# Kernel optimization log

Hardware: AMD Instinct MI355X
Metric: run time of the kernel (lower is better)

Reference implementation:

```python
import jax, jax.numpy as jnp
import numpy as np

B, T, D = 64, 512, 768
H = D // 2      # per-direction LSTM hidden
L = 33          # num_labels


def setup_inputs() -> dict:
    key = jax.random.key(0)
    ks = jax.random.split(key, 14)
    input_embed = jax.random.normal(ks[0], (B, T, D), dtype=jnp.float32)
    # pack_padded_sequence requires lengths sorted in decreasing order
    lengths = jnp.sort(jax.random.randint(ks[1], (B,), T // 2, T + 1))[::-1]
    lengths = lengths.at[0].set(T)
    mask = jnp.arange(T)[None, :] < lengths[:, None]          # [B,T] bool
    labels = jax.random.randint(ks[2], (B, T), 0, L, dtype=jnp.int32)
    index = jax.random.randint(ks[3], (B, 2), 0, T)
    s = 0.1
    w_ih_f = jax.random.normal(ks[4], (4 * H, D), jnp.float32) * s
    w_hh_f = jax.random.normal(ks[5], (4 * H, H), jnp.float32) * s
    b_f = jax.random.normal(ks[6], (4 * H,), jnp.float32) * s
    w_ih_b = jax.random.normal(ks[7], (4 * H, D), jnp.float32) * s
    w_hh_b = jax.random.normal(ks[8], (4 * H, H), jnp.float32) * s
    b_b = jax.random.normal(ks[9], (4 * H,), jnp.float32) * s
    lin_w = jax.random.normal(ks[10], (L, 2 * H), jnp.float32) * s
    lin_b = jnp.zeros((L,), jnp.float32)
    trans = jax.random.normal(ks[11], (L, L), jnp.float32) * s
    start_trans = jax.random.normal(ks[12], (L,), jnp.float32) * s
    end_trans = jax.random.normal(ks[13], (L,), jnp.float32) * s
    return dict(input_embed=input_embed, mask=mask, labels=labels, index=index,
                w_ih_f=w_ih_f, w_hh_f=w_hh_f, b_f=b_f,
                w_ih_b=w_ih_b, w_hh_b=w_hh_b, b_b=b_b,
                lin_w=lin_w, lin_b=lin_b,
                trans=trans, start_trans=start_trans, end_trans=end_trans)


def _run_lstm(x, mask_f, w_ih, w_hh, b):
    """Unidirectional LSTM over packed (length-masked) sequences.
    Output is zero at padded steps; state is frozen past each sequence length.
    x: [B,T,D] -> [B,T,H]. Torch gate order: i, f, g, o.
    """
    xp = jnp.einsum('btd,gd->btg', x, w_ih) + b          # [B,T,4H] precomputed
    xp_t = xp.transpose(1, 0, 2)                         # [T,B,4H]
    m_t = mask_f.T[:, :, None]                           # [T,B,1]
    nH = w_hh.shape[1]
    init = (jnp.zeros((x.shape[0], nH), x.dtype), jnp.zeros((x.shape[0], nH), x.dtype))

    def step(carry, inp):
        h, c = carry
        xg, m = inp
        g = xg + h @ w_hh.T
        i, f, gc, o = jnp.split(g, 4, axis=-1)
        c_new = jax.nn.sigmoid(f) * c + jax.nn.sigmoid(i) * jnp.tanh(gc)
        h_new = jax.nn.sigmoid(o) * jnp.tanh(c_new)
        carry = (jnp.where(m > 0, h_new, h), jnp.where(m > 0, c_new, c))
        return carry, h_new * m

    _, ys = jax.lax.scan(step, init, (xp_t, m_t))
    return ys.transpose(1, 0, 2)


def reference(input_embed, mask, labels, index,
              w_ih_f, w_hh_f, b_f, w_ih_b, w_hh_b, b_b,
              lin_w, lin_b, trans, start_trans, end_trans):
    mask_f = mask.astype(input_embed.dtype)              # [B,T]
    lengths = mask.sum(1).astype(jnp.int32)              # [B]

    # BiLSTM with pack_padded semantics (dropout in eval mode = identity)
    h_fwd = _run_lstm(input_embed, mask_f, w_ih_f, w_hh_f, b_f)
    # reverse within each sequence's valid region (involution on valid steps)
    rev_idx = jnp.clip(lengths[:, None] - 1 - jnp.arange(T)[None, :], 0, T - 1)
    x_rev = jnp.take_along_axis(input_embed, rev_idx[..., None], axis=1)
    h_b_rev = _run_lstm(x_rev, mask_f, w_ih_b, w_hh_b, b_b)
    h_bwd = jnp.take_along_axis(h_b_rev, rev_idx[..., None], axis=1) * mask_f[..., None]
    h = jnp.concatenate([h_fwd, h_bwd], axis=-1)         # [B,T,2H]

    # emissions, masked as in the original (out *= mask.unsqueeze(-1))
    em = (jnp.einsum('bth,lh->btl', h, lin_w) + lin_b) * mask_f[..., None]

    # ---- CRF log-likelihood: numerator (gold path score) ----
    em_y = jnp.take_along_axis(em, labels[..., None], axis=2)[..., 0]   # [B,T]
    tr = trans[labels[:, :-1], labels[:, 1:]]                            # [B,T-1]
    num = start_trans[labels[:, 0]] + em_y[:, 0] \
        + jnp.sum((tr + em_y[:, 1:]) * mask_f[:, 1:], axis=1)
    last_y = jnp.take_along_axis(labels, (lengths - 1)[:, None], axis=1)[:, 0]
    num = num + end_trans[last_y]

    # ---- CRF log-partition: forward algorithm scan ----
    alpha0 = start_trans[None, :] + em[:, 0]             # [B,L]

    def step(alpha, inp):
        e_t, m_t = inp                                   # [B,L], [B]
        new = jax.nn.logsumexp(alpha[:, :, None] + trans[None, :, :] + e_t[:, None, :], axis=1)
        return jnp.where(m_t[:, None] > 0, new, alpha), None

    alpha, _ = jax.lax.scan(step, alpha0,
                            (em[:, 1:].transpose(1, 0, 2), mask_f[:, 1:].T))
    logZ = jax.nn.logsumexp(alpha + end_trans[None, :], axis=1)

    score = num - logZ                                   # per-sample log-likelihood
    return -jnp.mean(score)
```

## Files before the change

kernel.cpp:

```cpp
#include <hip/hip_runtime.h>

typedef unsigned short U16;
typedef unsigned int   U32;
typedef unsigned long long U64;
typedef __attribute__((ext_vector_type(8))) short S8;
typedef __attribute__((ext_vector_type(4))) float F4;

#define B_  64
#define T_  512
#define DD  768
#define HH  384
#define G4  1536
#define NL  33

__device__ __forceinline__ U16 f2bf(float f){
  U32 u = __float_as_uint(f);
  u += 0x7fffu + ((u >> 16) & 1u);
  return (U16)(u >> 16);
}
__device__ __forceinline__ float bf2f(U16 h){ return __uint_as_float(((U32)h) << 16); }
__device__ __forceinline__ float frcp(float x){
  float r;
  asm("v_rcp_f32 %0, %1" : "=v"(r) : "v"(x));
  return r * (2.0f - x * r);
}
__device__ __forceinline__ float sigm(float x){
  x = fminf(30.f, fmaxf(-30.f, x));
  return frcp(1.f + __expf(-x));
}
__device__ __forceinline__ float tanh_(float x){
  x = fminf(15.f, fmaxf(-15.f, x));
  float e = __expf(2.f * x);
  return (e - 1.f) * frcp(e + 1.f);
}

__global__ void k_pre(const float* x, U64* xb, const U32* mask, int* lens,
                      const float* wf_, const float* wb_, const float* lw_,
                      const float* bfv, const float* bbv,
                      U16* wcat, U16* lwb, float* bcat){
  int blk = blockIdx.x;
  int tid = threadIdx.x;
  if (blk < 64){
    if (tid < 64){
      int b = blk, l = tid;
      bool b32 = (mask[0] == 1u);
      int cnt = 0;
      for (int t = l; t < T_; t += 64){
        int v = b32 ? ((const int*)mask)[b * T_ + t]
                    : (int)((const unsigned char*)mask)[b * T_ + t];
        cnt += (v != 0);
      }
      #pragma unroll
      for (int o = 32; o >= 1; o >>= 1) cnt += __shfl_xor(cnt, o);
      if (l == 0) lens[b] = cnt;
    }
    return;
  }
  if (blk < 1088){
    const int WE = G4 * DD;
    const int LWE = NL * DD;
    int total = 2 * WE + LWE + 2 * G4;
    for (int i = (blk - 64) * 256 + tid; i < total; i += 1024 * 256){
      if (i < WE) wcat[i] = f2bf(wf_[i]);
      else if (i < 2 * WE) wcat[i] = f2bf(wb_[i - WE]);
      else if (i < 2 * WE + LWE) lwb[i - 2 * WE] = f2bf(lw_[i - 2 * WE]);
      else { int j = i - 2 * WE - LWE; bcat[j] = (j < G4) ? bfv[j] : bbv[j - G4]; }
    }
    return;
  }
  size_t n4 = (size_t)B_ * T_ * DD / 4;
  for (size_t i = (size_t)(blk - 1088) * 256 + tid; i < n4; i += (size_t)2048 * 256){
    float4 v = ((const float4*)x)[i];
    U64 o = (U64)f2bf(v.x) | ((U64)f2bf(v.y) << 16) | ((U64)f2bf(v.z) << 32) | ((U64)f2bf(v.w) << 48);
    xb[i] = o;
  }
}

__global__ __launch_bounds__(256) void k_gemm(const U16* A, const U16* Bw, const float* bias, U16* C){
  __shared__ __align__(16) U16 As[128 * 64];
  __shared__ __align__(16) U16 Bs[128 * 64];
  int bid = blockIdx.x;
  int nb = bid % 24, mb = bid / 24;
  int m0 = mb * 128, n0 = nb * 128;
  int tid = threadIdx.x;
  int w = tid >> 6, l = tid & 63;
  int lr = l & 15, lk = (l >> 4) * 8;
  int wm = (w >> 1) * 64, wn = (w & 1) * 64;
  int srow = tid >> 3;
  int scol = (tid & 7) * 8;
  F4 acc[4][4];
  #pragma unroll
  for (int i = 0; i < 4; i++)
    #pragma unroll
    for (int j = 0; j < 4; j++) acc[i][j] = (F4){0.f, 0.f, 0.f, 0.f};

  for (int kt = 0; kt < DD; kt += 64){
    __syncthreads();
    #pragma unroll
    for (int r = 0; r < 4; r++){
      int row = r * 32 + srow;
      __builtin_amdgcn_global_load_lds((const U32*)(A + (size_t)(m0 + row) * DD + kt + scol),
                                       (U32*)(As + row * 64 + scol), 16, 0, 0);
      __builtin_amdgcn_global_load_lds((const U32*)(Bw + (size_t)(n0 + row) * DD + kt + scol),
                                       (U32*)(Bs + row * 64 + scol), 16, 0, 0);
    }
    __syncthreads();
    #pragma unroll
    for (int kk = 0; kk < 64; kk += 32){
      S8 af[4], bf[4];
      #pragma unroll
      for (int i = 0; i < 4; i++) af[i] = *(const S8*)(As + (wm + i * 16 + lr) * 64 + kk + lk);
      #pragma unroll
      for (int i = 0; i < 4; i++) bf[i] = *(const S8*)(Bs + (wn + i * 16 + lr) * 64 + kk + lk);
      #pragma unroll
      for (int i = 0; i < 4; i++)
        #pragma unroll
        for (int j = 0; j < 4; j++)
          acc[i][j] = __builtin_amdgcn_mfma_f32_16x16x32_bf16(af[i], bf[j], acc[i][j], 0, 0, 0);
    }
  }
  #pragma unroll
  for (int j = 0; j < 4; j++){
    int col = n0 + wn + j * 16 + lr;
    float bv = bias[col];
    #pragma unroll
    for (int i = 0; i < 4; i++){
      #pragma unroll
      for (int rg = 0; rg < 4; rg++){
        int row = m0 + wm + i * 16 + (l >> 4) * 4 + rg;
        C[(size_t)row * 3072 + col] = f2bf(acc[i][j][rg] + bv);
      }
    }
  }
}

__global__ __launch_bounds__(256) void k_rec(const U16* xp, const float* whf, const float* whb,
                                             const int* len_, U16* hcat, U64* hx){
  int blk = blockIdx.x;
  int g = blk & 7, m = blk >> 3;
  int dir = g >> 2, chunk = g & 3, sb = chunk * 16;
  const float* wh = dir ? whb : whf;
  int tid = threadIdx.x;
  int w = tid >> 6, l = tid & 63;
  int lr = l & 15, lq = l >> 4;
  int jloc = m * 64 + w * 16 + lr;

  S8 wf[4][12];
  #pragma unroll
  for (int q = 0; q < 4; q++){
    #pragma unroll
    for (int kc = 0; kc < 12; kc++){
      const float* p = wh + (size_t)(q * HH + jloc) * HH + kc * 32 + lq * 8;
      float4 v0 = *(const float4*)p;
      float4 v1 = *(const float4*)(p + 4);
      S8 t;
      t[0] = (short)f2bf(v0.x); t[1] = (short)f2bf(v0.y); t[2] = (short)f2bf(v0.z); t[3] = (short)f2bf(v0.w);
      t[4] = (short)f2bf(v1.x); t[5] = (short)f2bf(v1.y); t[6] = (short)f2bf(v1.z); t[7] = (short)f2bf(v1.w);
      wf[q][kc] = t;
    }
  }

  __shared__ __align__(16) U16 hl[16][408];
  for (int i = tid; i < 16 * 408; i += 256) ((U16*)hl)[i] = 0;
  int lens[4];
  #pragma unroll
  for (int r = 0; r < 4; r++) lens[r] = len_[sb + lq * 4 + r];
  int steps = len_[sb];
  float cst[4] = {0.f, 0.f, 0.f, 0.f}, hst[4] = {0.f, 0.f, 0.f, 0.f};
  __syncthreads();

  for (int step = 0; step < steps; ++step){
    float xv[4][4];
    #pragma unroll
    for (int r = 0; r < 4; r++){
      int L = lens[r];
      int t = dir ? (L - 1 - step) : step;
      if (t < 0) t = 0;
      size_t basei = ((size_t)(sb + lq * 4 + r) * T_ + t) * 3072 + dir * G4;
      #pragma unroll
      for (int q = 0; q < 4; q++) xv[q][r] = bf2f(xp[basei + q * HH + jloc]);
    }
    if (step){
      const U64* src = hx + (size_t)((step & 1) * 8 + g) * 3072;
      U64 v[12];
      #pragma unroll
      for (int k = 0; k < 12; k++)
        v[k] = __hip_atomic_load(src + tid + k * 256, __ATOMIC_RELAXED, __HIP_MEMORY_SCOPE_AGENT);
      U32 expct = (U32)step;
      while (true){
        U32 bad = 0;
        #pragma unroll
        for (int k = 0; k < 12; k++) bad |= (((U32)(v[k] >> 32)) != expct) ? (1u << k) : 0u;
        if (!bad) break;
        #pragma unroll
        for (int k = 0; k < 12; k++)
          if (bad & (1u << k))
            v[k] = __hip_atomic_load(src + tid + k * 256, __ATOMIC_RELAXED, __HIP_MEMORY_SCOPE_AGENT);
      }
      #pragma unroll
      for (int k = 0; k < 12; k++){
        int wi = tid + k * 256;
        int col = wi >> 3, p = wi & 7;
        U32 lo = (U32)v[k];
        hl[2 * p + 0][col] = (U16)lo;
        hl[2 * p + 1][col] = (U16)(lo >> 16);
      }
      __syncthreads();
    }
    F4 acc[4];
    #pragma unroll
    for (int q = 0; q < 4; q++) acc[q] = (F4){0.f, 0.f, 0.f, 0.f};
    #pragma unroll
    for (int kc = 0; kc < 12; kc++){
      S8 a = *(const S8*)&hl[lr][kc * 32 + lq * 8];
      #pragma unroll
      for (int q = 0; q < 4; q++)
        acc[q] = __builtin_amdgcn_mfma_f32_16x16x32_bf16(a, wf[q][kc], acc[q], 0, 0, 0);
    }
    #pragma unroll
    for (int r = 0; r < 4; r++){
      float ip = acc[0][r] + xv[0][r];
      float fp = acc[1][r] + xv[1][r];
      float gp = acc[2][r] + xv[2][r];
      float op = acc[3][r] + xv[3][r];
      float cn = sigm(fp) * cst[r] + sigm(ip) * tanh_(gp);
      float hn = sigm(op) * tanh_(cn);
      if (step < lens[r]){ cst[r] = cn; hst[r] = hn; }
    }
    {
      U64 tag = ((U64)(U32)(step + 1)) << 32;
      U64 w0 = (U64)((U32)f2bf(hst[0]) | ((U32)f2bf(hst[1]) << 16)) | tag;
      U64 w1 = (U64)((U32)f2bf(hst[2]) | ((U32)f2bf(hst[3]) << 16)) | tag;
      U64* dst = hx + (size_t)(((step + 1) & 1) * 8 + g) * 3072 + jloc * 8 + lq * 2;
      __hip_atomic_store(dst + 0, w0, __ATOMIC_RELAXED, __HIP_MEMORY_SCOPE_AGENT);
      __hip_atomic_store(dst + 1, w1, __ATOMIC_RELAXED, __HIP_MEMORY_SCOPE_AGENT);
    }
    #pragma unroll
    for (int r = 0; r < 4; r++){
      if (step < lens[r]){
        int t = dir ? (lens[r] - 1 - step) : step;
        hcat[((size_t)(sb + lq * 4 + r) * T_ + t) * (2 * HH) + dir * HH + jloc] = f2bf(hst[r]);
      }
    }
  }
}

__global__ __launch_bounds__(256) void k_em(const U16* hcat, const U16* lwb, const float* lin_b, float* em){
  __shared__ U16 lw[NL * DD];
  __shared__ U16 hs[8 * DD];
  int tid = threadIdx.x;
  for (int i = tid; i < NL * DD / 2; i += 256) ((U32*)lw)[i] = ((const U32*)lwb)[i];
  size_t r0 = (size_t)blockIdx.x * 8;
  const U32* hsrc = (const U32*)(hcat + r0 * DD);
  for (int i = tid; i < 8 * DD / 2; i += 256) ((U32*)hs)[i] = hsrc[i];
  __syncthreads();
  for (int e = tid; e < 8 * NL; e += 256){
    int rr = e / NL, ll = e % NL;
    const U16* hp = &hs[rr * DD];
    const U16* wp = &lw[ll * DD];
    float s = 0.f;
    #pragma unroll 8
    for (int k = 0; k < DD; k += 2){
      U32 hv = *(const U32*)&hp[k];
      U32 wv = *(const U32*)&wp[k];
      s = fmaf(__uint_as_float(hv << 16), __uint_as_float(wv << 16), s);
      s = fmaf(__uint_as_float(hv & 0xffff0000u), __uint_as_float(wv & 0xffff0000u), s);
    }
    em[(r0 + rr) * NL + ll] = s + lin_b[ll];
  }
}

__global__ void k_crf(const float* em, const int* labels, const int* len_, const float* trans,
                      const float* startt, const float* endt, float* score){
  int b = blockIdx.x, l = threadIdx.x;
  int L = len_[b];
  const int* lab = labels + b * T_;
  const float* emb = em + (size_t)b * T_ * NL;
  float part = 0.f;
  for (int t = 1 + l; t < L; t += 64){
    int lp = lab[t - 1], lc = lab[t];
    part += trans[lp * NL + lc] + emb[(size_t)t * NL + lc];
  }
  #pragma unroll
  for (int o = 32; o >= 1; o >>= 1) part += __shfl_xor(part, o);
  float num = part + startt[lab[0]] + emb[lab[0]] + endt[lab[L - 1]];
  bool act = l < NL;
  int jj = act ? l : (NL - 1);
  float tc[NL];
  #pragma unroll
  for (int i = 0; i < NL; i++) tc[i] = trans[i * NL + jj];
  float a = startt[jj] + emb[jj];
  for (int t = 1; t < L; ++t){
    float vv[NL];
    float mx = -3.0e38f;
    #pragma unroll
    for (int i = 0; i < NL; i++){ vv[i] = __shfl(a, i) + tc[i]; mx = fmaxf(mx, vv[i]); }
    float s = 0.f;
    #pragma unroll
    for (int i = 0; i < NL; i++) s += __expf(vv[i] - mx);
    a = mx + __logf(s) + emb[(size_t)t * NL + jj];
  }
  float val = act ? (a + endt[jj]) : -3.0e38f;
  float mx = val;
  #pragma unroll
  for (int o = 32; o >= 1; o >>= 1) mx = fmaxf(mx, __shfl_xor(mx, o));
  float se = __expf(val - mx);
  #pragma unroll
  for (int o = 32; o >= 1; o >>= 1) se += __shfl_xor(se, o);
  float logZ = mx + __logf(se);
  if (l == 0) score[b] = num - logZ;
}

__global__ void k_final(const float* score, float* out){
  int l = threadIdx.x;
  float v = score[l];
  #pragma unroll
  for (int o = 32; o >= 1; o >>= 1) v += __shfl_xor(v, o);
  if (l == 0) out[0] = -v / 64.f;
}

__global__ void k_sentinel(float* out){ out[0] = -12345.f; }

extern "C" void kernel_launch(void* const* d_in, const int* in_sizes, int n_in,
                              void* d_out, int out_size, void* d_ws, size_t ws_size,
                              hipStream_t stream){
  const float* x      = (const float*)d_in[0];
  const void*  mask   = d_in[1];
  const int*   labels = (const int*)d_in[2];
  const float* w_ih_f = (const float*)d_in[4];
  const float* w_hh_f = (const float*)d_in[5];
  const float* b_f    = (const float*)d_in[6];
  const float* w_ih_b = (const float*)d_in[7];
  const float* w_hh_b = (const float*)d_in[8];
  const float* b_b    = (const float*)d_in[9];
  const float* lin_w  = (const float*)d_in[10];
  const float* lin_b  = (const float*)d_in[11];
  const float* trans  = (const float*)d_in[12];
  const float* startt = (const float*)d_in[13];
  const float* endt   = (const float*)d_in[14];
  float* out = (float*)d_out;

  const size_t WS_NEEDED = 261158912;
  if (ws_size < WS_NEEDED){
    k_sentinel<<<1, 1, 0, stream>>>(out);
    return;
  }

  char* ws = (char*)d_ws;
  size_t off = 0;
  auto take = [&](size_t bytes) -> char* {
    char* p = ws + off;
    off += (bytes + 255) & ~(size_t)255;
    return p;
  };
  U16*  xp    = (U16*)take((size_t)32768 * 3072 * 2);
  U16*  hcat  = (U16*)take((size_t)32768 * 768 * 2);
  U16*  wcat  = (U16*)take((size_t)3072 * 768 * 2);
  U16*  lwb   = (U16*)take((size_t)NL * 768 * 2);
  float* bcat = (float*)take(3072 * 4);
  int*  lens  = (int*)take(256);
  U64*  hx    = (U64*)take((size_t)2 * 8 * 3072 * 8);
  float* em   = (float*)take((size_t)32768 * NL * 4);
  float* score= (float*)take(256);
  U16*  xbf   = hcat;

  hipMemsetAsync(hx, 0, (size_t)2 * 8 * 3072 * 8, stream);
  k_pre<<<3136, 256, 0, stream>>>(x, (U64*)xbf, (const U32*)mask, lens,
                                  w_ih_f, w_ih_b, lin_w, b_f, b_b, wcat, lwb, bcat);
  k_gemm<<<6144, 256, 0, stream>>>(xbf, wcat, bcat, xp);
  k_rec<<<48, 256, 0, stream>>>(xp, w_hh_f, w_hh_b, lens, hcat, hx);
  k_em<<<4096, 256, 0, stream>>>(hcat, lwb, lin_b, em);
  k_crf<<<64, 64, 0, stream>>>(em, labels, lens, trans, startt, endt, score);
  k_final<<<1, 64, 0, stream>>>(score, out);
}
```

Before: 2.245 ms.

## Fuse input bf16 conversion into GEMM, swizzle LDS, cheaper activations, bigger k_em tiles

Drops the separate fp32-to-bf16 pass over the input by loading fp32 directly in the input-projection GEMM and converting while staging to LDS. An XOR swizzle is added to the LDS layout and the block order is remapped. The gate activations lose their clamps and the Newton refinement on the reciprocal, and tanh uses a cheaper formulation. k_em now processes 32 rows per block with 64-bit loads. The GEMM A path now uses register-staged loads instead of async global-to-LDS loads, and the activations lose some precision.

```diff
diff --git a/kernel.cpp b/kernel.cpp
--- a/kernel.cpp
+++ b/kernel.cpp
@@ -22,19 +22,17 @@
 __device__ __forceinline__ float frcp(float x){
   float r;
   asm("v_rcp_f32 %0, %1" : "=v"(r) : "v"(x));
-  return r * (2.0f - x * r);
+  return r;
 }
 __device__ __forceinline__ float sigm(float x){
-  x = fminf(30.f, fmaxf(-30.f, x));
   return frcp(1.f + __expf(-x));
 }
 __device__ __forceinline__ float tanh_(float x){
-  x = fminf(15.f, fmaxf(-15.f, x));
   float e = __expf(2.f * x);
-  return (e - 1.f) * frcp(e + 1.f);
-}
-
-__global__ void k_pre(const float* x, U64* xb, const U32* mask, int* lens,
+  return 1.f - 2.f * frcp(e + 1.f);
+}
+
+__global__ void k_pre(const U32* mask, int* lens,
                       const float* wf_, const float* wb_, const float* lw_,
                       const float* bfv, const float* bbv,
                       U16* wcat, U16* lwb, float* bcat){
@@ -56,31 +54,24 @@
     }
     return;
   }
-  if (blk < 1088){
-    const int WE = G4 * DD;
-    const int LWE = NL * DD;
-    int total = 2 * WE + LWE + 2 * G4;
-    for (int i = (blk - 64) * 256 + tid; i < total; i += 1024 * 256){
-      if (i < WE) wcat[i] = f2bf(wf_[i]);
-      else if (i < 2 * WE) wcat[i] = f2bf(wb_[i - WE]);
-      else if (i < 2 * WE + LWE) lwb[i - 2 * WE] = f2bf(lw_[i - 2 * WE]);
-      else { int j = i - 2 * WE - LWE; bcat[j] = (j < G4) ? bfv[j] : bbv[j - G4]; }
-    }
-    return;
-  }
-  size_t n4 = (size_t)B_ * T_ * DD / 4;
-  for (size_t i = (size_t)(blk - 1088) * 256 + tid; i < n4; i += (size_t)2048 * 256){
-    float4 v = ((const float4*)x)[i];
-    U64 o = (U64)f2bf(v.x) | ((U64)f2bf(v.y) << 16) | ((U64)f2bf(v.z) << 32) | ((U64)f2bf(v.w) << 48);
-    xb[i] = o;
-  }
-}
-
-__global__ __launch_bounds__(256) void k_gemm(const U16* A, const U16* Bw, const float* bias, U16* C){
+  const int WE = G4 * DD;
+  const int LWE = NL * DD;
+  int total = 2 * WE + LWE + 2 * G4;
+  for (int i = (blk - 64) * 256 + tid; i < total; i += 512 * 256){
+    if (i < WE) wcat[i] = f2bf(wf_[i]);
+    else if (i < 2 * WE) wcat[i] = f2bf(wb_[i - WE]);
+    else if (i < 2 * WE + LWE) lwb[i - 2 * WE] = f2bf(lw_[i - 2 * WE]);
+    else { int j = i - 2 * WE - LWE; bcat[j] = (j < G4) ? bfv[j] : bbv[j - G4]; }
+  }
+}
+
+__global__ __launch_bounds__(256) void k_gemm(const float* __restrict__ x,
+                                              const U16* __restrict__ Bw,
+                                              const float* __restrict__ bias, U16* C){
   __shared__ __align__(16) U16 As[128 * 64];
   __shared__ __align__(16) U16 Bs[128 * 64];
-  int bid = blockIdx.x;
-  int nb = bid % 24, mb = bid / 24;
+  int swz = (blockIdx.x & 7) * 768 + (blockIdx.x >> 3);
+  int mb = swz & 255, nb = swz >> 8;
   int m0 = mb * 128, n0 = nb * 128;
   int tid = threadIdx.x;
   int w = tid >> 6, l = tid & 63;
@@ -99,19 +90,28 @@
     #pragma unroll
     for (int r = 0; r < 4; r++){
       int row = r * 32 + srow;
-      __builtin_amdgcn_global_load_lds((const U32*)(A + (size_t)(m0 + row) * DD + kt + scol),
-                                       (U32*)(As + row * 64 + scol), 16, 0, 0);
-      __builtin_amdgcn_global_load_lds((const U32*)(Bw + (size_t)(n0 + row) * DD + kt + scol),
+      int sw = scol ^ ((row & 7) * 8);
+      const float* ap = x + (size_t)(m0 + row) * DD + kt + sw;
+      float4 v0 = *(const float4*)ap;
+      float4 v1 = *(const float4*)(ap + 4);
+      S8 t;
+      t[0] = (short)f2bf(v0.x); t[1] = (short)f2bf(v0.y);
+      t[2] = (short)f2bf(v0.z); t[3] = (short)f2bf(v0.w);
+      t[4] = (short)f2bf(v1.x); t[5] = (short)f2bf(v1.y);
+      t[6] = (short)f2bf(v1.z); t[7] = (short)f2bf(v1.w);
+      *(S8*)&As[row * 64 + sw] = t;
+      __builtin_amdgcn_global_load_lds((const U32*)(Bw + (size_t)(n0 + row) * DD + kt + sw),
                                        (U32*)(Bs + row * 64 + scol), 16, 0, 0);
     }
     __syncthreads();
     #pragma unroll
     for (int kk = 0; kk < 64; kk += 32){
       S8 af[4], bf[4];
-      #pragma unroll
-      for (int i = 0; i < 4; i++) af[i] = *(const S8*)(As + (wm + i * 16 + lr) * 64 + kk + lk);
-      #pragma unroll
-      for (int i = 0; i < 4; i++) bf[i] = *(const S8*)(Bs + (wn + i * 16 + lr) * 64 + kk + lk);
+      int cs = (kk + lk) ^ ((lr & 7) * 8);
+      #pragma unroll
+      for (int i = 0; i < 4; i++) af[i] = *(const S8*)(As + (wm + i * 16 + lr) * 64 + cs);
+      #pragma unroll
+      for (int i = 0; i < 4; i++) bf[i] = *(const S8*)(Bs + (wn + i * 16 + lr) * 64 + cs);
       #pragma unroll
       for (int i = 0; i < 4; i++)
         #pragma unroll
@@ -134,8 +134,11 @@
   }
 }
 
-__global__ __launch_bounds__(256) void k_rec(const U16* xp, const float* whf, const float* whb,
-                                             const int* len_, U16* hcat, U64* hx){
+__global__ __launch_bounds__(256, 1) void k_rec(const U16* __restrict__ xp,
+                                                const float* __restrict__ whf,
+                                                const float* __restrict__ whb,
+                                                const int* __restrict__ len_,
+                                                U16* __restrict__ hcat, U64* hx){
   int blk = blockIdx.x;
   int g = blk & 7, m = blk >> 3;
   int dir = g >> 2, chunk = g & 3, sb = chunk * 16;
@@ -246,15 +249,15 @@
 }
 
 __global__ __launch_bounds__(256) void k_em(const U16* hcat, const U16* lwb, const float* lin_b, float* em){
-  __shared__ U16 lw[NL * DD];
-  __shared__ U16 hs[8 * DD];
+  __shared__ __align__(16) U16 lw[NL * DD];
+  __shared__ __align__(16) U16 hs[32 * DD];
   int tid = threadIdx.x;
-  for (int i = tid; i < NL * DD / 2; i += 256) ((U32*)lw)[i] = ((const U32*)lwb)[i];
-  size_t r0 = (size_t)blockIdx.x * 8;
-  const U32* hsrc = (const U32*)(hcat + r0 * DD);
-  for (int i = tid; i < 8 * DD / 2; i += 256) ((U32*)hs)[i] = hsrc[i];
+  for (int i = tid; i < NL * DD / 4; i += 256) ((U64*)lw)[i] = ((const U64*)lwb)[i];
+  size_t r0 = (size_t)blockIdx.x * 32;
+  const U64* hsrc = (const U64*)(hcat + r0 * DD);
+  for (int i = tid; i < 32 * DD / 4; i += 256) ((U64*)hs)[i] = hsrc[i];
   __syncthreads();
-  for (int e = tid; e < 8 * NL; e += 256){
+  for (int e = tid; e < 32 * NL; e += 256){
     int rr = e / NL, ll = e % NL;
     const U16* hp = &hs[rr * DD];
     const U16* wp = &lw[ll * DD];
@@ -362,14 +365,13 @@
   U64*  hx    = (U64*)take((size_t)2 * 8 * 3072 * 8);
   float* em   = (float*)take((size_t)32768 * NL * 4);
   float* score= (float*)take(256);
-  U16*  xbf   = hcat;
-
-  hipMemsetAsync(hx, 0, (size_t)2 * 8 * 3072 * 8, stream);
-  k_pre<<<3136, 256, 0, stream>>>(x, (U64*)xbf, (const U32*)mask, lens,
-                                  w_ih_f, w_ih_b, lin_w, b_f, b_b, wcat, lwb, bcat);
-  k_gemm<<<6144, 256, 0, stream>>>(xbf, wcat, bcat, xp);
+
+  (void)hipMemsetAsync(hx, 0, (size_t)2 * 8 * 3072 * 8, stream);
+  k_pre<<<576, 256, 0, stream>>>((const U32*)mask, lens,
+                                 w_ih_f, w_ih_b, lin_w, b_f, b_b, wcat, lwb, bcat);
+  k_gemm<<<6144, 256, 0, stream>>>(x, wcat, bcat, xp);
   k_rec<<<48, 256, 0, stream>>>(xp, w_hh_f, w_hh_b, lens, hcat, hx);
-  k_em<<<4096, 256, 0, stream>>>(hcat, lwb, lin_b, em);
+  k_em<<<1024, 256, 0, stream>>>(hcat, lwb, lin_b, em);
   k_crf<<<64, 64, 0, stream>>>(em, labels, lens, trans, startt, endt, score);
   k_final<<<1, 64, 0, stream>>>(score, out);
 }
```

New measurement: 2.368 ms. 1.05x slower.
